# Optimization experiments

Measured on AMD Instinct MI355X. Metric: run time of the kernel, lower is better.

Reference implementation:

```python
import jax, jax.numpy as jnp
import numpy as np

K = 8192   # num_embeddings
D = 256    # embedding_dim


def setup_inputs() -> dict:
    key = jax.random.key(0)
    k1, k2 = jax.random.split(key)
    inputs = jax.random.normal(k1, (8, 4096, D), dtype=jnp.float32)
    # torch init: uniform_(-1/num_embeddings, 1/num_embeddings)
    embeddings_weight = jax.random.uniform(
        k2, (K, D), dtype=jnp.float32, minval=-1.0 / K, maxval=1.0 / K
    )
    return {"inputs": inputs, "embeddings_weight": embeddings_weight}


def reference(inputs, embeddings_weight):
    in_shape = inputs.shape
    flat = inputs.reshape(-1, D)                      # [N, D]
    distances = (
        jnp.sum(flat * flat, axis=1, keepdims=True)   # [N, 1]
        + jnp.sum(embeddings_weight * embeddings_weight, axis=1)  # [K]
        - 2.0 * jnp.matmul(flat, embeddings_weight.T)             # [N, K]
    )
    encoding_indices = jnp.argmin(distances, axis=1)  # [N] int
    # one-hot @ W is mathematically a row gather of W
    quantized = jnp.take(embeddings_weight, encoding_indices, axis=0).reshape(in_shape)
    return quantized, encoding_indices
```

## Files before the change

### kernel.cpp

```cpp
#include <hip/hip_runtime.h>
#include <cfloat>


#define DDIM 256

typedef int   i32x8  __attribute__((ext_vector_type(8)));
typedef float f32x16 __attribute__((ext_vector_type(16)));

__global__ __launch_bounds__(256) void vq_prep_w(
    const float* __restrict__ w, float* __restrict__ wn,
    unsigned char* __restrict__ wb8) {
    __shared__ float rows[32 * 260];
    const int tid = threadIdx.x;
    const int r0 = blockIdx.x * 32;

    for (int idx = tid; idx < 32 * 64; idx += 256) {
        int r = idx >> 6, c4 = idx & 63;
        *(float4*)&rows[r * 260 + c4 * 4] =
            *(const float4*)(w + (size_t)(r0 + r) * DDIM + c4 * 4);
    }
    __syncthreads();
    {
        const int row = (tid >> 6) * 8 + ((tid & 63) >> 3), j = tid & 7;
        const float* a = &rows[row * 260];
        float half[2];
#pragma unroll
        for (int h = 0; h < 2; ++h) {
            const float* b = a + h * 128 + j;
            float r = __fmul_rn(b[0], b[0]);
#pragma unroll
            for (int t = 1; t < 16; ++t)
                r = __fadd_rn(r, __fmul_rn(b[8 * t], b[8 * t]));
            float p = __fadd_rn(r, __shfl_xor(r, 1, 64));
            p = __fadd_rn(p, __shfl_xor(p, 2, 64));
            p = __fadd_rn(p, __shfl_xor(p, 4, 64));
            half[h] = p;
        }
        if (j == 0) wn[r0 + row] = __fadd_rn(half[0], half[1]);
    }
    for (int idx = tid; idx < 32 * 16; idx += 256) {
        int r = idx >> 4, s = idx & 15;
        const float* p = &rows[r * 260 + s * 16];
        unsigned q[4];
#pragma unroll
        for (int m = 0; m < 4; ++m) {
            unsigned v = (unsigned)__builtin_amdgcn_cvt_pk_fp8_f32(
                p[m * 4 + 0] * -8192.f, p[m * 4 + 1] * -8192.f, 0, false);
            v = (unsigned)__builtin_amdgcn_cvt_pk_fp8_f32(
                p[m * 4 + 2] * -8192.f, p[m * 4 + 3] * -8192.f, (int)v, true);
            q[m] = v;
        }
        *(uint4*)(wb8 + (size_t)(r0 + r) * DDIM + s * 16) =
            make_uint4(q[0], q[1], q[2], q[3]);
    }
}

__global__ __launch_bounds__(256, 2) void vq_score(
    const float* __restrict__ x, const unsigned char* __restrict__ wb8,
    unsigned* __restrict__ cand) {
    __shared__ __align__(16) unsigned char Ws[2][32768];
    const int tid = threadIdx.x;
    const int wave = tid >> 6, lane = tid & 63;
    const int h = lane >> 5, c32 = lane & 31;
    const int wc = wave;
    const int rowBase = blockIdx.x * 64;

    i32x8 af[2][4];
#pragma unroll
    for (int rt = 0; rt < 2; ++rt) {
        const float* xr = x + (size_t)(rowBase + rt * 32 + c32) * DDIM;
#pragma unroll
        for (int ks = 0; ks < 4; ++ks) {
            const float4* p = (const float4*)(xr + ks * 64 + h * 32);
            union { int d[8]; i32x8 v; } u;
#pragma unroll
            for (int m = 0; m < 8; ++m) {
                float4 f = p[m];
                unsigned v = (unsigned)__builtin_amdgcn_cvt_pk_fp8_f32(
                    f.x, f.y, 0, false);
                v = (unsigned)__builtin_amdgcn_cvt_pk_fp8_f32(
                    f.z, f.w, (int)v, true);
                u.d[m] = (int)v;
            }
            af[rt][ks] = u.v;
        }
    }

    unsigned sOfs[8], ldsOfs[8];
#pragma unroll
    for (int i = 0; i < 8; ++i) {
        int slot = wave * 8 + i;
        int col  = slot * 4 + (lane >> 4);
        int gsrc = (lane & 15) ^ (col & 15);
        sOfs[i]   = (unsigned)(col * 256 + gsrc * 16);
        ldsOfs[i] = (unsigned)(slot * 1024);
    }

    unsigned s0[2][16], s1[2][16];
#pragma unroll
    for (int a = 0; a < 2; ++a)
#pragma unroll
        for (int r = 0; r < 16; ++r) { s0[a][r] = 0xFFFFFFFFu; s1[a][r] = 0xFFFFFFFFu; }

    const int bcol = wc * 32 + c32, cs = bcol & 15;
    int bofs[4][2];
#pragma unroll
    for (int ks = 0; ks < 4; ++ks) {
        int gb = ks * 4 + h * 2;
        bofs[ks][0] = bcol * 256 + ((gb)     ^ cs) * 16;
        bofs[ks][1] = bcol * 256 + ((gb + 1) ^ cs) * 16;
    }

    auto stage = [&](int kt, int buf) {
        const unsigned char* g = wb8 + (size_t)kt * 32768;
#pragma unroll
        for (int i = 0; i < 8; ++i)
            __builtin_amdgcn_global_load_lds(
                (const __attribute__((address_space(1))) unsigned int*)(g + sOfs[i]),
                (__attribute__((address_space(3))) unsigned int*)(&Ws[buf][ldsOfs[i]]),
                16, 0, 0);
    };

    stage(0, 0);
    for (int kt = 0; kt < 64; ++kt) {
        const int cur = kt & 1;
        __syncthreads();
        if (kt + 1 < 64) stage(kt + 1, cur ^ 1);

        f32x16 acc[2];
#pragma unroll
        for (int rt = 0; rt < 2; ++rt)
#pragma unroll
            for (int r = 0; r < 16; ++r) acc[rt][r] = 128.0f;
#pragma unroll
        for (int ks = 0; ks < 4; ++ks) {
            union { uint4 q[2]; i32x8 v; } b;
            b.q[0] = *(const uint4*)&Ws[cur][bofs[ks][0]];
            b.q[1] = *(const uint4*)&Ws[cur][bofs[ks][1]];
#pragma unroll
            for (int rt = 0; rt < 2; ++rt)
                acc[rt] = __builtin_amdgcn_mfma_scale_f32_32x32x64_f8f6f4(
                    af[rt][ks], b.v, acc[rt], 0, 0,
                    0, 0x7F7F7F7F, 0, 0x7F7F7F7F);
        }
        const unsigned colv = (unsigned)(kt * 128 + bcol);
#pragma unroll
        for (int rt = 0; rt < 2; ++rt)
#pragma unroll
            for (int r = 0; r < 16; ++r) {
                unsigned key = (__float_as_uint(acc[rt][r]) & 0xFFFFE000u) | colv;
                unsigned a0 = s0[rt][r];
                unsigned mx = key > a0 ? key : a0;
                s1[rt][r] = mx < s1[rt][r] ? mx : s1[rt][r];
                s0[rt][r] = key < a0 ? key : a0;
            }
    }

    __syncthreads();
    unsigned* ms = (unsigned*)Ws;
#pragma unroll
    for (int rt = 0; rt < 2; ++rt)
#pragma unroll
        for (int r = 0; r < 16; ++r) {
            int rloc = rt * 32 + (r & 3) + 8 * (r >> 2) + 4 * h;
            *(uint2*)&ms[rloc * 256 + bcol * 2] = make_uint2(s0[rt][r], s1[rt][r]);
        }
    __syncthreads();
    if (tid < 64) {
        const uint4* rowk = (const uint4*)(ms + tid * 256);
        unsigned best[8];
#pragma unroll
        for (int i = 0; i < 8; ++i) best[i] = 0xFFFFFFFFu;
        for (int i = 0; i < 64; ++i) {
            uint4 qv = rowk[(i + tid) & 63];
            unsigned kk[4] = {qv.x, qv.y, qv.z, qv.w};
#pragma unroll
            for (int e = 0; e < 4; ++e) {
                unsigned key = kk[e];
                if (key < best[7]) {
                    best[7] = key;
#pragma unroll
                    for (int j = 7; j > 0; --j)
                        if (best[j] < best[j - 1]) {
                            unsigned t = best[j]; best[j] = best[j - 1]; best[j - 1] = t;
                        }
                }
            }
        }
        unsigned* out = cand + (size_t)(rowBase + tid) * 8;
#pragma unroll
        for (int i = 0; i < 8; ++i) out[i] = best[i];
    }
}

__global__ __launch_bounds__(256) void vq_rescore_write(
    const float* __restrict__ x, const float* __restrict__ w,
    const float* __restrict__ wn, const unsigned* __restrict__ cand,
    float* __restrict__ outq, float* __restrict__ outi) {
    __shared__ int winners[32];
    const int tid = threadIdx.x;
    const int lr = tid >> 3, cc = tid & 7;
    const int row = blockIdx.x * 32 + lr;

    int k = (int)(cand[(size_t)row * 8 + cc] & 0x1FFFu);
    const float* xr = x + (size_t)row * DDIM;
    const float* wr = w + (size_t)k * DDIM;
    float dot = 0.f;
    float half[2];
#pragma unroll
    for (int hh = 0; hh < 2; ++hh) {
        float r[8];
#pragma unroll
        for (int t = 0; t < 16; ++t) {
            const int d = hh * 128 + t * 8;
            float4 xa = *(const float4*)(xr + d);
            float4 xb = *(const float4*)(xr + d + 4);
            float4 wa = *(const float4*)(wr + d);
            float4 wb = *(const float4*)(wr + d + 4);
            dot = __fmaf_rn(xa.x, wa.x, dot); dot = __fmaf_rn(xa.y, wa.y, dot);
            dot = __fmaf_rn(xa.z, wa.z, dot); dot = __fmaf_rn(xa.w, wa.w, dot);
            dot = __fmaf_rn(xb.x, wb.x, dot); dot = __fmaf_rn(xb.y, wb.y, dot);
            dot = __fmaf_rn(xb.z, wb.z, dot); dot = __fmaf_rn(xb.w, wb.w, dot);
            if (t == 0) {
                r[0] = __fmul_rn(xa.x, xa.x); r[1] = __fmul_rn(xa.y, xa.y);
                r[2] = __fmul_rn(xa.z, xa.z); r[3] = __fmul_rn(xa.w, xa.w);
                r[4] = __fmul_rn(xb.x, xb.x); r[5] = __fmul_rn(xb.y, xb.y);
                r[6] = __fmul_rn(xb.z, xb.z); r[7] = __fmul_rn(xb.w, xb.w);
            } else {
                r[0] = __fadd_rn(r[0], __fmul_rn(xa.x, xa.x));
                r[1] = __fadd_rn(r[1], __fmul_rn(xa.y, xa.y));
                r[2] = __fadd_rn(r[2], __fmul_rn(xa.z, xa.z));
                r[3] = __fadd_rn(r[3], __fmul_rn(xa.w, xa.w));
                r[4] = __fadd_rn(r[4], __fmul_rn(xb.x, xb.x));
                r[5] = __fadd_rn(r[5], __fmul_rn(xb.y, xb.y));
                r[6] = __fadd_rn(r[6], __fmul_rn(xb.w == xb.w ? xb.z : xb.z, xb.z));
                r[7] = __fadd_rn(r[7], __fmul_rn(xb.w, xb.w));
            }
        }
        half[hh] = __fadd_rn(__fadd_rn(__fadd_rn(r[0], r[1]), __fadd_rn(r[2], r[3])),
                             __fadd_rn(__fadd_rn(r[4], r[5]), __fadd_rn(r[6], r[7])));
    }
    float x2v = __fadd_rn(half[0], half[1]);
    float dv = __fsub_rn(__fadd_rn(x2v, wn[k]), __fmul_rn(2.0f, dot));
#pragma unroll
    for (int m = 1; m < 8; m <<= 1) {
        float od = __shfl_xor(dv, m, 64);
        int   ok = __shfl_xor(k,  m, 64);
        if (od < dv || (od == dv && ok < k)) { dv = od; k = ok; }
    }
    if (cc == 0) winners[lr] = k;
    __syncthreads();
    if (tid < 32) outi[blockIdx.x * 32 + tid] = (float)winners[tid];
    for (int u = tid; u < 32 * 64; u += 256) {
        int r = u >> 6, c4 = u & 63;
        *reinterpret_cast<float4*>(outq + (size_t)(blockIdx.x * 32 + r) * DDIM + c4 * 4) =
            *reinterpret_cast<const float4*>(w + (size_t)winners[r] * DDIM + c4 * 4);
    }
}

extern "C" void kernel_launch(void* const* d_in, const int* in_sizes, int n_in,
                              void* d_out, int out_size, void* d_ws, size_t ws_size,
                              hipStream_t stream) {
    const float* x = (const float*)d_in[0];
    const float* w = (const float*)d_in[1];
    const int N = in_sizes[0] / DDIM;
    const int K = in_sizes[1] / DDIM;
    float* outq = (float*)d_out;
    float* outi = outq + (size_t)N * DDIM;

    unsigned char* wb8 = (unsigned char*)d_ws;
    float* wn = (float*)(wb8 + (size_t)K * DDIM);
    unsigned* cand = (unsigned*)(wn + K);

    hipLaunchKernelGGL(vq_prep_w, dim3(K / 32), dim3(256), 0, stream, w, wn, wb8);
    hipLaunchKernelGGL(vq_score, dim3(N / 64), dim3(256), 0, stream, x, wb8, cand);
    hipLaunchKernelGGL(vq_rescore_write, dim3(N / 32), dim3(256), 0, stream,
                       x, w, wn, cand, outq, outi);
}
```

Baseline: 256.1 us.

## Split codebook tiles into half-K stages with 4-buffer software pipeline and med3 top-2

Each 128-column codebook tile is split into two half-depth stages across a four-buffer ring, and the per-tile barrier is replaced with explicit vmcnt waits. The main loop is software-pipelined so the top-2 selection of one tile's accumulators is interleaved with the MFMAs of the next tile, with raised wave priority around the MFMA blocks. The second-best update is collapsed into a single v_med3_u32. This aims to hide global-to-LDS latency and selection ALU work behind matrix math, at the cost of more accumulator registers and fragile hand-counted waitcnt logic.

```diff
diff --git a/kernel.cpp b/kernel.cpp
--- a/kernel.cpp
+++ b/kernel.cpp
@@ -55,15 +55,48 @@
     }
 }
 
+
+#define WBARi(n) asm volatile("s_waitcnt vmcnt(" #n ")\n\ts_barrier" ::: "memory")
+
+#define INIT128(C) { _Pragma("unroll") for (int r_ = 0; r_ < 16; ++r_) (C)[r_] = 128.0f; }
+
+#define SEL16(P, rt, pkt) { \
+    const unsigned colv_ = (unsigned)((pkt) * 128 + bcol); \
+    _Pragma("unroll") for (int r_ = 0; r_ < 16; ++r_) { \
+        unsigned key_ = (__float_as_uint((P)[r_]) & 0xFFFFE000u) | colv_; \
+        unsigned a0_ = s0[rt][r_]; \
+        unsigned m1_; \
+        asm("v_med3_u32 %0, %1, %2, %3" \
+            : "=v"(m1_) : "v"(key_), "v"(a0_), "v"(s1[rt][r_])); \
+        s1[rt][r_] = m1_; \
+        s0[rt][r_] = key_ < a0_ ? key_ : a0_; \
+    } }
+
+#define KS2(bufi, KA, KB, C0, C1) do { \
+    union { uint4 q[2]; i32x8 v; } b_; \
+    b_.q[0] = *(const uint4*)(wsb + (bufi) * 16384 + rb[0]); \
+    b_.q[1] = *(const uint4*)(wsb + (bufi) * 16384 + rb[1]); \
+    C0 = __builtin_amdgcn_mfma_scale_f32_32x32x64_f8f6f4( \
+        af[0][KA], b_.v, C0, 0, 0, 0, 0x7F7F7F7F, 0, 0x7F7F7F7F); \
+    C1 = __builtin_amdgcn_mfma_scale_f32_32x32x64_f8f6f4( \
+        af[1][KA], b_.v, C1, 0, 0, 0, 0x7F7F7F7F, 0, 0x7F7F7F7F); \
+    b_.q[0] = *(const uint4*)(wsb + (bufi) * 16384 + rb[2]); \
+    b_.q[1] = *(const uint4*)(wsb + (bufi) * 16384 + rb[3]); \
+    C0 = __builtin_amdgcn_mfma_scale_f32_32x32x64_f8f6f4( \
+        af[0][KB], b_.v, C0, 0, 0, 0, 0x7F7F7F7F, 0, 0x7F7F7F7F); \
+    C1 = __builtin_amdgcn_mfma_scale_f32_32x32x64_f8f6f4( \
+        af[1][KB], b_.v, C1, 0, 0, 0, 0x7F7F7F7F, 0, 0x7F7F7F7F); \
+  } while (0)
+
 __global__ __launch_bounds__(256, 2) void vq_score(
     const float* __restrict__ x, const unsigned char* __restrict__ wb8,
     unsigned* __restrict__ cand) {
-    __shared__ __align__(16) unsigned char Ws[2][32768];
+    __shared__ __align__(16) unsigned char Ws[4][16384];
     const int tid = threadIdx.x;
     const int wave = tid >> 6, lane = tid & 63;
     const int h = lane >> 5, c32 = lane & 31;
-    const int wc = wave;
     const int rowBase = blockIdx.x * 64;
+    const unsigned char* wsb = (const unsigned char*)&Ws[0][0];
 
     i32x8 af[2][4];
 #pragma unroll
@@ -85,76 +118,75 @@
             af[rt][ks] = u.v;
         }
     }
-
-    unsigned sOfs[8], ldsOfs[8];
-#pragma unroll
-    for (int i = 0; i < 8; ++i) {
-        int slot = wave * 8 + i;
-        int col  = slot * 4 + (lane >> 4);
-        int gsrc = (lane & 15) ^ (col & 15);
-        sOfs[i]   = (unsigned)(col * 256 + gsrc * 16);
-        ldsOfs[i] = (unsigned)(slot * 1024);
-    }
-
-    unsigned s0[2][16], s1[2][16];
-#pragma unroll
-    for (int a = 0; a < 2; ++a)
-#pragma unroll
-        for (int r = 0; r < 16; ++r) { s0[a][r] = 0xFFFFFFFFu; s1[a][r] = 0xFFFFFFFFu; }
-
-    const int bcol = wc * 32 + c32, cs = bcol & 15;
-    int bofs[4][2];
-#pragma unroll
-    for (int ks = 0; ks < 4; ++ks) {
-        int gb = ks * 4 + h * 2;
-        bofs[ks][0] = bcol * 256 + ((gb)     ^ cs) * 16;
-        bofs[ks][1] = bcol * 256 + ((gb + 1) ^ cs) * 16;
-    }
-
-    auto stage = [&](int kt, int buf) {
-        const unsigned char* g = wb8 + (size_t)kt * 32768;
-#pragma unroll
-        for (int i = 0; i < 8; ++i)
+    asm volatile("s_waitcnt vmcnt(0)" ::: "memory");
+
+    const unsigned laneTerm =
+        (unsigned)((lane >> 3) * 256 + (((lane & 7) ^ (lane >> 3)) * 16));
+    auto stage = [&](int hh) {
+        const unsigned char* g = wb8 + (size_t)(hh >> 1) * 32768 +
+                                 (hh & 1) * 128 + wave * 8192 + laneTerm;
+        const int bb = (hh & 3) * 16384 + wave * 4096;
+#pragma unroll
+        for (int i = 0; i < 4; ++i)
             __builtin_amdgcn_global_load_lds(
-                (const __attribute__((address_space(1))) unsigned int*)(g + sOfs[i]),
-                (__attribute__((address_space(3))) unsigned int*)(&Ws[buf][ldsOfs[i]]),
+                (const __attribute__((address_space(1))) unsigned int*)(g + i * 2048),
+                (__attribute__((address_space(3))) unsigned int*)(
+                    &Ws[0][0] + bb + i * 1024),
                 16, 0, 0);
     };
 
-    stage(0, 0);
-    for (int kt = 0; kt < 64; ++kt) {
-        const int cur = kt & 1;
-        __syncthreads();
-        if (kt + 1 < 64) stage(kt + 1, cur ^ 1);
-
-        f32x16 acc[2];
-#pragma unroll
-        for (int rt = 0; rt < 2; ++rt)
-#pragma unroll
-            for (int r = 0; r < 16; ++r) acc[rt][r] = 128.0f;
-#pragma unroll
-        for (int ks = 0; ks < 4; ++ks) {
-            union { uint4 q[2]; i32x8 v; } b;
-            b.q[0] = *(const uint4*)&Ws[cur][bofs[ks][0]];
-            b.q[1] = *(const uint4*)&Ws[cur][bofs[ks][1]];
-#pragma unroll
-            for (int rt = 0; rt < 2; ++rt)
-                acc[rt] = __builtin_amdgcn_mfma_scale_f32_32x32x64_f8f6f4(
-                    af[rt][ks], b.v, acc[rt], 0, 0,
-                    0, 0x7F7F7F7F, 0, 0x7F7F7F7F);
-        }
-        const unsigned colv = (unsigned)(kt * 128 + bcol);
-#pragma unroll
-        for (int rt = 0; rt < 2; ++rt)
-#pragma unroll
-            for (int r = 0; r < 16; ++r) {
-                unsigned key = (__float_as_uint(acc[rt][r]) & 0xFFFFE000u) | colv;
-                unsigned a0 = s0[rt][r];
-                unsigned mx = key > a0 ? key : a0;
-                s1[rt][r] = mx < s1[rt][r] ? mx : s1[rt][r];
-                s0[rt][r] = key < a0 ? key : a0;
-            }
-    }
+    const int bcol = wave * 32 + c32, cs = bcol & 7;
+    unsigned rb[4];
+    {
+        const int e0 = h * 2;
+        rb[0] = (unsigned)(bcol * 128 + ((e0 ^ cs) * 16));
+        rb[1] = (unsigned)(bcol * 128 + (((e0 + 1) ^ cs) * 16));
+        rb[2] = (unsigned)(bcol * 128 + (((e0 + 4) ^ cs) * 16));
+        rb[3] = (unsigned)(bcol * 128 + (((e0 + 5) ^ cs) * 16));
+    }
+
+    unsigned s0[2][16], s1[2][16];
+#pragma unroll
+    for (int a = 0; a < 2; ++a)
+#pragma unroll
+        for (int r = 0; r < 16; ++r) { s0[a][r] = 0xFFFFFFFFu; s1[a][r] = 0xFFFFFFFFu; }
+
+    f32x16 cA0, cA1, cB0, cB1;
+
+    stage(0); stage(1); stage(2);
+
+    INIT128(cB0); INIT128(cB1);
+    WBARi(8); stage(3);
+    __builtin_amdgcn_s_setprio(1); KS2(0, 0, 1, cB0, cB1); __builtin_amdgcn_s_setprio(0);
+    WBARi(8); stage(4);
+    __builtin_amdgcn_s_setprio(1); KS2(1, 2, 3, cB0, cB1); __builtin_amdgcn_s_setprio(0);
+
+    for (int kt = 1; kt < 63; kt += 2) {
+        INIT128(cA0); INIT128(cA1);
+        WBARi(8); stage(2 * kt + 3);
+        __builtin_amdgcn_s_setprio(1); KS2(2, 0, 1, cA0, cA1); __builtin_amdgcn_s_setprio(0);
+        SEL16(cB0, 0, kt - 1);
+        WBARi(8); stage(2 * kt + 4);
+        __builtin_amdgcn_s_setprio(1); KS2(3, 2, 3, cA0, cA1); __builtin_amdgcn_s_setprio(0);
+        SEL16(cB1, 1, kt - 1);
+        INIT128(cB0); INIT128(cB1);
+        WBARi(8); stage(2 * kt + 5);
+        __builtin_amdgcn_s_setprio(1); KS2(0, 0, 1, cB0, cB1); __builtin_amdgcn_s_setprio(0);
+        SEL16(cA0, 0, kt);
+        WBARi(8); if (kt < 61) stage(2 * kt + 6);
+        __builtin_amdgcn_s_setprio(1); KS2(1, 2, 3, cB0, cB1); __builtin_amdgcn_s_setprio(0);
+        SEL16(cA1, 1, kt);
+    }
+
+    INIT128(cA0); INIT128(cA1);
+    WBARi(4);
+    __builtin_amdgcn_s_setprio(1); KS2(2, 0, 1, cA0, cA1); __builtin_amdgcn_s_setprio(0);
+    SEL16(cB0, 0, 62);
+    WBARi(0);
+    __builtin_amdgcn_s_setprio(1); KS2(3, 2, 3, cA0, cA1); __builtin_amdgcn_s_setprio(0);
+    SEL16(cB1, 1, 62);
+    SEL16(cA0, 0, 63);
+    SEL16(cA1, 1, 63);
 
     __syncthreads();
     unsigned* ms = (unsigned*)Ws;
```

After: 273.0 us. 1.07x slower.

## Replace block barriers with per-wave vmcnt waits in the fp8 scoring loop

Applied to the files above, without the earlier changes.

Each wave stages into LDS exactly the 32 codebook columns it later reads. The main loop therefore drops __syncthreads and instead waits on its own outstanding global_load_lds with s_waitcnt vmcnt, peeling the last iteration so it can wait for zero. It also raises wave priority around the MFMA block and adds an explicit vmcnt(0) after the prologue x loads. This removes the block-wide barrier stall each tile, but correctness now depends on the per-wave ownership of LDS slots and on hand-placed wait counts.

```diff
diff --git a/kernel.cpp b/kernel.cpp
--- a/kernel.cpp
+++ b/kernel.cpp
@@ -54,6 +54,24 @@
             make_uint4(q[0], q[1], q[2], q[3]);
     }
 }
+
+
+#define VWAIT(n) do { \
+    asm volatile("s_waitcnt vmcnt(" #n ")" ::: "memory"); \
+    __builtin_amdgcn_sched_barrier(0); \
+  } while (0)
+
+#define INIT128(C) { _Pragma("unroll") for (int r_ = 0; r_ < 16; ++r_) (C)[r_] = 128.0f; }
+
+#define SEL16(P, rt, pkt) { \
+    const unsigned colv_ = (unsigned)((pkt) * 128 + bcol); \
+    _Pragma("unroll") for (int r_ = 0; r_ < 16; ++r_) { \
+        unsigned key_ = (__float_as_uint((P)[r_]) & 0xFFFFE000u) | colv_; \
+        unsigned a0_ = s0[rt][r_]; \
+        unsigned mx_ = key_ > a0_ ? key_ : a0_; \
+        s1[rt][r_] = mx_ < s1[rt][r_] ? mx_ : s1[rt][r_]; \
+        s0[rt][r_] = key_ < a0_ ? key_ : a0_; \
+    } }
 
 __global__ __launch_bounds__(256, 2) void vq_score(
     const float* __restrict__ x, const unsigned char* __restrict__ wb8,
@@ -62,8 +80,8 @@
     const int tid = threadIdx.x;
     const int wave = tid >> 6, lane = tid & 63;
     const int h = lane >> 5, c32 = lane & 31;
-    const int wc = wave;
     const int rowBase = blockIdx.x * 64;
+    const unsigned char* wsb = (const unsigned char*)&Ws[0][0];
 
     i32x8 af[2][4];
 #pragma unroll
@@ -85,6 +103,7 @@
             af[rt][ks] = u.v;
         }
     }
+    asm volatile("s_waitcnt vmcnt(0)" ::: "memory");
 
     unsigned sOfs[8], ldsOfs[8];
 #pragma unroll
@@ -95,14 +114,18 @@
         sOfs[i]   = (unsigned)(col * 256 + gsrc * 16);
         ldsOfs[i] = (unsigned)(slot * 1024);
     }
-
-    unsigned s0[2][16], s1[2][16];
-#pragma unroll
-    for (int a = 0; a < 2; ++a)
-#pragma unroll
-        for (int r = 0; r < 16; ++r) { s0[a][r] = 0xFFFFFFFFu; s1[a][r] = 0xFFFFFFFFu; }
-
-    const int bcol = wc * 32 + c32, cs = bcol & 15;
+    auto stage = [&](int kt, unsigned tgl) {
+        const unsigned char* g = wb8 + (size_t)kt * 32768;
+#pragma unroll
+        for (int i = 0; i < 8; ++i)
+            __builtin_amdgcn_global_load_lds(
+                (const __attribute__((address_space(1))) unsigned int*)(g + sOfs[i]),
+                (__attribute__((address_space(3))) unsigned int*)(
+                    &Ws[0][0] + tgl + ldsOfs[i]),
+                16, 0, 0);
+    };
+
+    const int bcol = wave * 32 + c32, cs = bcol & 15;
     int bofs[4][2];
 #pragma unroll
     for (int ks = 0; ks < 4; ++ks) {
@@ -111,49 +134,53 @@
         bofs[ks][1] = bcol * 256 + ((gb + 1) ^ cs) * 16;
     }
 
-    auto stage = [&](int kt, int buf) {
-        const unsigned char* g = wb8 + (size_t)kt * 32768;
-#pragma unroll
-        for (int i = 0; i < 8; ++i)
-            __builtin_amdgcn_global_load_lds(
-                (const __attribute__((address_space(1))) unsigned int*)(g + sOfs[i]),
-                (__attribute__((address_space(3))) unsigned int*)(&Ws[buf][ldsOfs[i]]),
-                16, 0, 0);
-    };
+    unsigned s0[2][16], s1[2][16];
+#pragma unroll
+    for (int a = 0; a < 2; ++a)
+#pragma unroll
+        for (int r = 0; r < 16; ++r) { s0[a][r] = 0xFFFFFFFFu; s1[a][r] = 0xFFFFFFFFu; }
+
+    f32x16 acc0, acc1;
 
     stage(0, 0);
-    for (int kt = 0; kt < 64; ++kt) {
-        const int cur = kt & 1;
-        __syncthreads();
-        if (kt + 1 < 64) stage(kt + 1, cur ^ 1);
-
-        f32x16 acc[2];
-#pragma unroll
-        for (int rt = 0; rt < 2; ++rt)
-#pragma unroll
-            for (int r = 0; r < 16; ++r) acc[rt][r] = 128.0f;
+
+    for (int kt = 0; kt < 63; ++kt) {
+        const unsigned tgl = (unsigned)(kt & 1) << 15;
+        stage(kt + 1, tgl ^ 32768u);
+        INIT128(acc0); INIT128(acc1);
+        VWAIT(8);
+        __builtin_amdgcn_s_setprio(1);
 #pragma unroll
         for (int ks = 0; ks < 4; ++ks) {
-            union { uint4 q[2]; i32x8 v; } b;
-            b.q[0] = *(const uint4*)&Ws[cur][bofs[ks][0]];
-            b.q[1] = *(const uint4*)&Ws[cur][bofs[ks][1]];
-#pragma unroll
-            for (int rt = 0; rt < 2; ++rt)
-                acc[rt] = __builtin_amdgcn_mfma_scale_f32_32x32x64_f8f6f4(
-                    af[rt][ks], b.v, acc[rt], 0, 0,
-                    0, 0x7F7F7F7F, 0, 0x7F7F7F7F);
-        }
-        const unsigned colv = (unsigned)(kt * 128 + bcol);
-#pragma unroll
-        for (int rt = 0; rt < 2; ++rt)
-#pragma unroll
-            for (int r = 0; r < 16; ++r) {
-                unsigned key = (__float_as_uint(acc[rt][r]) & 0xFFFFE000u) | colv;
-                unsigned a0 = s0[rt][r];
-                unsigned mx = key > a0 ? key : a0;
-                s1[rt][r] = mx < s1[rt][r] ? mx : s1[rt][r];
-                s0[rt][r] = key < a0 ? key : a0;
-            }
+            union { uint4 q[2]; i32x8 v; } b_;
+            b_.q[0] = *(const uint4*)(wsb + tgl + bofs[ks][0]);
+            b_.q[1] = *(const uint4*)(wsb + tgl + bofs[ks][1]);
+            acc0 = __builtin_amdgcn_mfma_scale_f32_32x32x64_f8f6f4(
+                af[0][ks], b_.v, acc0, 0, 0, 0, 0x7F7F7F7F, 0, 0x7F7F7F7F);
+            acc1 = __builtin_amdgcn_mfma_scale_f32_32x32x64_f8f6f4(
+                af[1][ks], b_.v, acc1, 0, 0, 0, 0x7F7F7F7F, 0, 0x7F7F7F7F);
+        }
+        __builtin_amdgcn_s_setprio(0);
+        SEL16(acc0, 0, kt);
+        SEL16(acc1, 1, kt);
+    }
+    {
+        INIT128(acc0); INIT128(acc1);
+        VWAIT(0);
+        __builtin_amdgcn_s_setprio(1);
+#pragma unroll
+        for (int ks = 0; ks < 4; ++ks) {
+            union { uint4 q[2]; i32x8 v; } b_;
+            b_.q[0] = *(const uint4*)(wsb + 32768 + bofs[ks][0]);
+            b_.q[1] = *(const uint4*)(wsb + 32768 + bofs[ks][1]);
+            acc0 = __builtin_amdgcn_mfma_scale_f32_32x32x64_f8f6f4(
+                af[0][ks], b_.v, acc0, 0, 0, 0, 0x7F7F7F7F, 0, 0x7F7F7F7F);
+            acc1 = __builtin_amdgcn_mfma_scale_f32_32x32x64_f8f6f4(
+                af[1][ks], b_.v, acc1, 0, 0, 0, 0x7F7F7F7F, 0, 0x7F7F7F7F);
+        }
+        __builtin_amdgcn_s_setprio(0);
+        SEL16(acc0, 0, 63);
+        SEL16(acc1, 1, 63);
     }
 
     __syncthreads();
```

Result: faster. 249.9 us (-2.5%).

## Load codebook fragments directly from global memory instead of LDS staging

Applied to the files above, without the earlier changes.

The score kernel stops staging fp8 codebook tiles into double-buffered shared memory through global_load_lds and barriers. Each lane now loads its B fragments straight from global (L2-resident) memory into registers, with a two-deep register prefetch. The block row tile is halved from 64 to 32 rows, so twice as many blocks launch and occupancy hints rise to 3 blocks per CU, and MFMA groups are wrapped in s_setprio. This removes the per-tile barriers and LDS traffic, but each codebook byte is fetched once per 32 rows instead of once per 64, which doubles global/L2 reads.

```diff
diff --git a/kernel.cpp b/kernel.cpp
--- a/kernel.cpp
+++ b/kernel.cpp
@@ -55,20 +55,51 @@
     }
 }
 
-__global__ __launch_bounds__(256, 2) void vq_score(
+
+#define INIT128(C) { _Pragma("unroll") for (int r_ = 0; r_ < 16; ++r_) (C)[r_] = 128.0f; }
+
+#define SEL16(P, pkt) { \
+    const unsigned colv_ = (unsigned)((pkt) * 128 + bcol); \
+    _Pragma("unroll") for (int r_ = 0; r_ < 16; ++r_) { \
+        unsigned key_ = (__float_as_uint((P)[r_]) & 0xFFFFE000u) | colv_; \
+        unsigned a0_ = s0[r_]; \
+        unsigned mx_ = key_ > a0_ ? key_ : a0_; \
+        s1[r_] = mx_ < s1[r_] ? mx_ : s1[r_]; \
+        s0[r_] = key_ < a0_ ? key_ : a0_; \
+    } }
+
+#define LOADB(dst, kt) { \
+    _Pragma("unroll") for (int ks_ = 0; ks_ < 4; ++ks_) { \
+        dst[ks_].q[0] = *(const uint4*)(wB + (kt) * 32768 + ks_ * 64); \
+        dst[ks_].q[1] = *(const uint4*)(wB + (kt) * 32768 + ks_ * 64 + 16); \
+    } }
+
+#define MFMA4(B) do { \
+    __builtin_amdgcn_s_setprio(1); \
+    acc = __builtin_amdgcn_mfma_scale_f32_32x32x64_f8f6f4( \
+        af[0], B[0].v, acc, 0, 0, 0, 0x7F7F7F7F, 0, 0x7F7F7F7F); \
+    acc = __builtin_amdgcn_mfma_scale_f32_32x32x64_f8f6f4( \
+        af[1], B[1].v, acc, 0, 0, 0, 0x7F7F7F7F, 0, 0x7F7F7F7F); \
+    acc = __builtin_amdgcn_mfma_scale_f32_32x32x64_f8f6f4( \
+        af[2], B[2].v, acc, 0, 0, 0, 0x7F7F7F7F, 0, 0x7F7F7F7F); \
+    acc = __builtin_amdgcn_mfma_scale_f32_32x32x64_f8f6f4( \
+        af[3], B[3].v, acc, 0, 0, 0, 0x7F7F7F7F, 0, 0x7F7F7F7F); \
+    __builtin_amdgcn_s_setprio(0); \
+  } while (0)
+
+__global__ __launch_bounds__(256, 3) void vq_score(
     const float* __restrict__ x, const unsigned char* __restrict__ wb8,
     unsigned* __restrict__ cand) {
-    __shared__ __align__(16) unsigned char Ws[2][32768];
+    __shared__ unsigned ms[32 * 256];
     const int tid = threadIdx.x;
     const int wave = tid >> 6, lane = tid & 63;
     const int h = lane >> 5, c32 = lane & 31;
-    const int wc = wave;
-    const int rowBase = blockIdx.x * 64;
-
-    i32x8 af[2][4];
-#pragma unroll
-    for (int rt = 0; rt < 2; ++rt) {
-        const float* xr = x + (size_t)(rowBase + rt * 32 + c32) * DDIM;
+    const int rowBase = blockIdx.x * 32;
+    const int bcol = wave * 32 + c32;
+
+    i32x8 af[4];
+    {
+        const float* xr = x + (size_t)(rowBase + c32) * DDIM;
 #pragma unroll
         for (int ks = 0; ks < 4; ++ks) {
             const float4* p = (const float4*)(xr + ks * 64 + h * 32);
@@ -82,91 +113,38 @@
                     f.z, f.w, (int)v, true);
                 u.d[m] = (int)v;
             }
-            af[rt][ks] = u.v;
-        }
-    }
-
-    unsigned sOfs[8], ldsOfs[8];
-#pragma unroll
-    for (int i = 0; i < 8; ++i) {
-        int slot = wave * 8 + i;
-        int col  = slot * 4 + (lane >> 4);
-        int gsrc = (lane & 15) ^ (col & 15);
-        sOfs[i]   = (unsigned)(col * 256 + gsrc * 16);
-        ldsOfs[i] = (unsigned)(slot * 1024);
-    }
-
-    unsigned s0[2][16], s1[2][16];
-#pragma unroll
-    for (int a = 0; a < 2; ++a)
-#pragma unroll
-        for (int r = 0; r < 16; ++r) { s0[a][r] = 0xFFFFFFFFu; s1[a][r] = 0xFFFFFFFFu; }
-
-    const int bcol = wc * 32 + c32, cs = bcol & 15;
-    int bofs[4][2];
-#pragma unroll
-    for (int ks = 0; ks < 4; ++ks) {
-        int gb = ks * 4 + h * 2;
-        bofs[ks][0] = bcol * 256 + ((gb)     ^ cs) * 16;
-        bofs[ks][1] = bcol * 256 + ((gb + 1) ^ cs) * 16;
-    }
-
-    auto stage = [&](int kt, int buf) {
-        const unsigned char* g = wb8 + (size_t)kt * 32768;
-#pragma unroll
-        for (int i = 0; i < 8; ++i)
-            __builtin_amdgcn_global_load_lds(
-                (const __attribute__((address_space(1))) unsigned int*)(g + sOfs[i]),
-                (__attribute__((address_space(3))) unsigned int*)(&Ws[buf][ldsOfs[i]]),
-                16, 0, 0);
-    };
-
-    stage(0, 0);
-    for (int kt = 0; kt < 64; ++kt) {
-        const int cur = kt & 1;
-        __syncthreads();
-        if (kt + 1 < 64) stage(kt + 1, cur ^ 1);
-
-        f32x16 acc[2];
-#pragma unroll
-        for (int rt = 0; rt < 2; ++rt)
-#pragma unroll
-            for (int r = 0; r < 16; ++r) acc[rt][r] = 128.0f;
-#pragma unroll
-        for (int ks = 0; ks < 4; ++ks) {
-            union { uint4 q[2]; i32x8 v; } b;
-            b.q[0] = *(const uint4*)&Ws[cur][bofs[ks][0]];
-            b.q[1] = *(const uint4*)&Ws[cur][bofs[ks][1]];
-#pragma unroll
-            for (int rt = 0; rt < 2; ++rt)
-                acc[rt] = __builtin_amdgcn_mfma_scale_f32_32x32x64_f8f6f4(
-                    af[rt][ks], b.v, acc[rt], 0, 0,
-                    0, 0x7F7F7F7F, 0, 0x7F7F7F7F);
-        }
-        const unsigned colv = (unsigned)(kt * 128 + bcol);
-#pragma unroll
-        for (int rt = 0; rt < 2; ++rt)
-#pragma unroll
-            for (int r = 0; r < 16; ++r) {
-                unsigned key = (__float_as_uint(acc[rt][r]) & 0xFFFFE000u) | colv;
-                unsigned a0 = s0[rt][r];
-                unsigned mx = key > a0 ? key : a0;
-                s1[rt][r] = mx < s1[rt][r] ? mx : s1[rt][r];
-                s0[rt][r] = key < a0 ? key : a0;
-            }
-    }
-
+            af[ks] = u.v;
+        }
+    }
+
+    const unsigned char* wB = wb8 + (size_t)bcol * 256 + h * 32;
+
+    unsigned s0[16], s1[16];
+#pragma unroll
+    for (int r = 0; r < 16; ++r) { s0[r] = 0xFFFFFFFFu; s1[r] = 0xFFFFFFFFu; }
+
+    f32x16 acc;
+    union Bu { uint4 q[2]; i32x8 v; };
+    Bu bE[4], bO[4];
+
+    LOADB(bE, 0);
+    for (int kt = 0; kt < 64; kt += 2) {
+        LOADB(bO, kt + 1);
+        INIT128(acc);
+        MFMA4(bE);
+        SEL16(acc, kt);
+        if (kt + 2 < 64) LOADB(bE, kt + 2);
+        INIT128(acc);
+        MFMA4(bO);
+        SEL16(acc, kt + 1);
+    }
+
+    for (int r = 0; r < 16; ++r) {
+        int rloc = (r & 3) + 8 * (r >> 2) + 4 * h;
+        *(uint2*)&ms[rloc * 256 + bcol * 2] = make_uint2(s0[r], s1[r]);
+    }
     __syncthreads();
-    unsigned* ms = (unsigned*)Ws;
-#pragma unroll
-    for (int rt = 0; rt < 2; ++rt)
-#pragma unroll
-        for (int r = 0; r < 16; ++r) {
-            int rloc = rt * 32 + (r & 3) + 8 * (r >> 2) + 4 * h;
-            *(uint2*)&ms[rloc * 256 + bcol * 2] = make_uint2(s0[rt][r], s1[rt][r]);
-        }
-    __syncthreads();
-    if (tid < 64) {
+    if (tid < 32) {
         const uint4* rowk = (const uint4*)(ms + tid * 256);
         unsigned best[8];
 #pragma unroll
@@ -273,7 +251,7 @@
     unsigned* cand = (unsigned*)(wn + K);
 
     hipLaunchKernelGGL(vq_prep_w, dim3(K / 32), dim3(256), 0, stream, w, wn, wb8);
-    hipLaunchKernelGGL(vq_score, dim3(N / 64), dim3(256), 0, stream, x, wb8, cand);
+    hipLaunchKernelGGL(vq_score, dim3(N / 32), dim3(256), 0, stream, x, wb8, cand);
     hipLaunchKernelGGL(vq_rescore_write, dim3(N / 32), dim3(256), 0, stream,
                        x, w, wn, cand, outq, outi);
 }
```

After: 561.5 us. 119% more time.
